# Optimization experiments

Measured on AMD Instinct MI355X. Metric: run time of the kernel, lower is better.

The kernel has to match this reference:

```python
import jax, jax.numpy as jnp
import numpy as np

THRESHOLD = 0.35
NEGPOS = 7
VAR0, VAR1 = 0.1, 0.2


def point_form(boxes):
    # (cx,cy,w,h) -> (x1,y1,x2,y2)
    return jnp.concatenate([boxes[:, :2] - boxes[:, 2:] / 2,
                            boxes[:, :2] + boxes[:, 2:] / 2], axis=1)


def jaccard(box_a, box_b):
    # box_a: [T,4], box_b: [P,4] in point form -> IoU [T,P]
    max_xy = jnp.minimum(box_a[:, None, 2:], box_b[None, :, 2:])
    min_xy = jnp.maximum(box_a[:, None, :2], box_b[None, :, :2])
    wh = jnp.clip(max_xy - min_xy, 0.0)
    inter = wh[..., 0] * wh[..., 1]
    area_a = ((box_a[:, 2] - box_a[:, 0]) * (box_a[:, 3] - box_a[:, 1]))[:, None]
    area_b = ((box_b[:, 2] - box_b[:, 0]) * (box_b[:, 3] - box_b[:, 1]))[None, :]
    return inter / (area_a + area_b - inter)


def encode(matched, priors):
    # matched: [P,4] point form, priors: [P,4] center form
    g_cxcy = ((matched[:, :2] + matched[:, 2:]) / 2 - priors[:, :2]) / (VAR0 * priors[:, 2:])
    g_wh = jnp.log((matched[:, 2:] - matched[:, :2]) / priors[:, 2:]) / VAR1
    return jnp.concatenate([g_cxcy, g_wh], axis=1)


def encode_landm(matched, priors):
    m = matched.reshape(-1, 5, 2)                       # [P,5,2]
    g = (m - priors[:, None, :2]) / (VAR0 * priors[:, None, 2:])
    return g.reshape(-1, 10)


def match_one(truths, labels, landms, priors):
    # truths [T,4], labels [T], landms [T,10], priors [P,4]
    overlaps = jaccard(truths, point_form(priors))       # [T,P]
    best_prior_idx = jnp.argmax(overlaps, axis=1)        # [T]
    best_truth_overlap = overlaps.max(axis=0)            # [P]
    best_truth_idx = jnp.argmax(overlaps, axis=0)        # [P]
    best_truth_overlap = best_truth_overlap.at[best_prior_idx].set(2.0)
    def body(j, bti):
        return bti.at[best_prior_idx[j]].set(j)
    best_truth_idx = jax.lax.fori_loop(0, truths.shape[0], body, best_truth_idx)
    conf = jnp.where(best_truth_overlap < THRESHOLD, 0.0, labels[best_truth_idx])
    loc = encode(truths[best_truth_idx], priors)
    landm = encode_landm(landms[best_truth_idx], priors)
    return loc, conf, landm


def smooth_l1(p, t):
    d = jnp.abs(p - t)
    return jnp.where(d < 1.0, 0.5 * d * d, d - 0.5)


def reference(loc_data, conf_data, landm_data, priors, targets):
    num, num_priors, _ = loc_data.shape
    truths = targets[:, :, :4]
    landms = targets[:, :, 4:14]
    labels = targets[:, :, 14]
    loc_t, conf_f, landm_t = jax.vmap(match_one, in_axes=(0, 0, 0, None))(
        truths, labels, landms, priors)
    conf_t = conf_f.astype(jnp.int32)                    # [num, P]

    poslands = conf_t > 0
    loss_landm = jnp.sum(smooth_l1(landm_data, landm_t) * poslands[..., None])

    pos = conf_t != 0
    loss_l = jnp.sum(smooth_l1(loc_data, loc_t) * pos[..., None])

    conf_t = jnp.where(pos, 1, conf_t)
    # per-prior CE: logsumexp - logit[target]
    ce = jax.nn.logsumexp(conf_data, axis=-1) - \
        jnp.take_along_axis(conf_data, conf_t[..., None], axis=-1)[..., 0]

    # hard negative mining: rank negatives by CE, keep top negpos*num_pos
    loss_rank = jnp.where(pos, 0.0, ce)
    loss_idx = jnp.argsort(-loss_rank, axis=1)
    idx_rank = jnp.argsort(loss_idx, axis=1)
    num_pos = pos.sum(axis=1)
    num_neg = jnp.clip(NEGPOS * num_pos, 0, num_priors - 1)
    neg = idx_rank < num_neg[:, None]

    sel = pos | neg
    loss_c = jnp.sum(ce * sel)

    N = jnp.maximum(num_pos.sum().astype(loc_data.dtype), 1.0)
    N1 = jnp.maximum(poslands.sum().astype(loc_data.dtype), 1.0)
    return loss_l / N, loss_c / N, loss_landm / N1


def setup_inputs() -> dict:
    key = jax.random.key(0)
    ks = jax.random.split(key, 8)
    N, T, P = 16, 48, 65536
    loc_data = jax.random.normal(ks[0], (N, P, 4), dtype=jnp.float32) * 0.1
    conf_data = jax.random.normal(ks[1], (N, P, 2), dtype=jnp.float32)
    landm_data = jax.random.normal(ks[2], (N, P, 10), dtype=jnp.float32) * 0.1
    # priors in (cx,cy,w,h), w,h > 0
    pc = jax.random.uniform(ks[3], (P, 2), minval=0.05, maxval=0.95)
    pwh = jax.random.uniform(ks[4], (P, 2), minval=0.04, maxval=0.3)
    priors = jnp.concatenate([pc, pwh], axis=1).astype(jnp.float32)
    # GT boxes: valid point-form (x1<x2, y1<y2)
    tc = jax.random.uniform(ks[5], (N, T, 2), minval=0.1, maxval=0.9)
    twh = jax.random.uniform(ks[6], (N, T, 2), minval=0.05, maxval=0.3)
    boxes = jnp.concatenate([tc - twh / 2, tc + twh / 2], axis=-1)
    lm = jax.random.uniform(ks[7], (N, T, 10))
    labels = jnp.ones((N, T, 1))
    targets = jnp.concatenate([boxes, lm, labels], axis=-1).astype(jnp.float32)
    return {"loc_data": loc_data, "conf_data": conf_data,
            "landm_data": landm_data, "priors": priors, "targets": targets}
```

## Files before the change

kernel.cpp:

```cpp
#include <hip/hip_runtime.h>

#define NP 65536
#define NT 48
#define TH 0.35f
#define PPT 2
#define KC_BX 128

#define PACKED_OFF 0
#define HIST_OFF   6144
#define NCPY 4
#define ZERO_BYTES 530432
#define NEGSUM_OFF 530432
#define PART_OFF   531456
#define LRANK_OFF  596992

__device__ __forceinline__ float sml1(float d) {
    float a = fabsf(d);
    return a < 1.f ? 0.5f * a * a : a - 0.5f;
}

__global__ __launch_bounds__(256) void kA(const float* __restrict__ priors,
                                          const float* __restrict__ targets,
                                          unsigned long long* __restrict__ packed) {
    const int chunk = blockIdx.x, tg = blockIdx.y, b = blockIdx.z;
    const float* tb = targets + ((size_t)b * NT + tg * 8) * 15;
    float tx1[8], ty1[8], tx2[8], ty2[8], ta[8];
#pragma unroll
    for (int j = 0; j < 8; j++) {
        tx1[j] = tb[j * 15 + 0]; ty1[j] = tb[j * 15 + 1];
        tx2[j] = tb[j * 15 + 2]; ty2[j] = tb[j * 15 + 3];
        ta[j] = (tx2[j] - tx1[j]) * (ty2[j] - ty1[j]);
    }
    const int pbase = chunk * 4096;
    float bi[8], bu[8]; unsigned int bp_[8];
#pragma unroll
    for (int j = 0; j < 8; j++) { bi[j] = 0.f; bu[j] = 1.f; bp_[j] = pbase + threadIdx.x; }
    const float4* P4 = reinterpret_cast<const float4*>(priors);
    for (int i = threadIdx.x; i < 4096; i += 256) {
        const int p = pbase + i;
        const float4 q = P4[p];
        const float px1 = q.x - q.z * 0.5f, py1 = q.y - q.w * 0.5f;
        const float px2 = q.x + q.z * 0.5f, py2 = q.y + q.w * 0.5f;
        const float areaB = (px2 - px1) * (py2 - py1);
#pragma unroll
        for (int j = 0; j < 8; j++) {
            float w = fminf(tx2[j], px2) - fmaxf(tx1[j], px1);
            float h = fminf(ty2[j], py2) - fmaxf(ty1[j], py1);
            w = fmaxf(w, 0.f); h = fmaxf(h, 0.f);
            float inter = w * h;
            float u = ta[j] + areaB - inter;
            if (inter * bu[j] > bi[j] * u) { bi[j] = inter; bu[j] = u; bp_[j] = (unsigned int)p; }
        }
    }
    __shared__ unsigned long long red[4][8];
    const int lane = threadIdx.x & 63, w = threadIdx.x >> 6;
#pragma unroll
    for (int j = 0; j < 8; j++) {
        float iou = bi[j] * __builtin_amdgcn_rcpf(bu[j]);
        unsigned long long key =
            ((unsigned long long)__float_as_uint(iou) << 32) | (unsigned long long)(~bp_[j]);
        for (int s = 32; s > 0; s >>= 1) {
            unsigned long long o = __shfl_down(key, s, 64);
            if (o > key) key = o;
        }
        if (lane == 0) red[w][j] = key;
    }
    __syncthreads();
    if (threadIdx.x < 8) {
        unsigned long long m = red[0][threadIdx.x];
#pragma unroll
        for (int i = 1; i < 4; i++) { unsigned long long o = red[i][threadIdx.x]; if (o > m) m = o; }
        atomicMax(&packed[(b * 6 + tg) * 8 + threadIdx.x], m);
    }
}

__global__ __launch_bounds__(256) void kC(
    const float* __restrict__ loc_data, const float* __restrict__ conf_data,
    const float* __restrict__ landm_data, const float* __restrict__ priors,
    const float* __restrict__ targets, const unsigned long long* __restrict__ packed,
    float* __restrict__ lrank, unsigned int* __restrict__ hist1c,
    float* __restrict__ part) {
    const int b = blockIdx.y;
    const int bx = blockIdx.x;
    const int p0 = (bx * 256 + threadIdx.x) * PPT;
    const int blockBase = bx * 256 * PPT;

    __shared__ float4 tbox[NT];
    __shared__ float tlab[NT];
    __shared__ float tlm[NT][10];
    __shared__ unsigned int hist[2048];
    __shared__ int ccnt;
    __shared__ int clp[NT], clt[NT];

    if (threadIdx.x == 0) ccnt = 0;
#pragma unroll
    for (int i = 0; i < 8; i++) hist[threadIdx.x + i * 256] = 0;
    for (int i = threadIdx.x; i < NT * 15; i += 256) {
        int t = i / 15, f = i - t * 15;
        float v = targets[((size_t)b * NT + t) * 15 + f];
        if (f < 4) reinterpret_cast<float*>(&tbox[t])[f] = v;
        else if (f < 14) tlm[t][f - 4] = v;
        else tlab[t] = v;
    }
    __syncthreads();
    if (threadIdx.x < NT) {
        int t = threadIdx.x;
        int cp = (int)(~(unsigned int)(packed[(b * 6 + (t >> 3)) * 8 + (t & 7)] & 0xFFFFFFFFull));
        if ((unsigned int)(cp - blockBase) < (unsigned int)(256 * PPT)) {
            int idx = atomicAdd(&ccnt, 1);
            clp[idx] = cp; clt[idx] = t;
        }
    }
    __syncthreads();

    float px1[PPT], py1[PPT], px2[PPT], py2[PPT], aB[PPT];
    float bi[PPT], bu[PPT]; int bt[PPT];
#pragma unroll
    for (int j = 0; j < PPT; j++) {
        float4 q = reinterpret_cast<const float4*>(priors)[p0 + j];
        px1[j] = q.x - q.z * 0.5f; py1[j] = q.y - q.w * 0.5f;
        px2[j] = q.x + q.z * 0.5f; py2[j] = q.y + q.w * 0.5f;
        aB[j] = (px2[j] - px1[j]) * (py2[j] - py1[j]);
        bi[j] = 0.f; bu[j] = 1.f; bt[j] = 0;
    }

    for (int t = 0; t < NT; t++) {
        float4 tb = tbox[t];
        float ta = (tb.z - tb.x) * (tb.w - tb.y);
#pragma unroll
        for (int j = 0; j < PPT; j++) {
            float w = fminf(tb.z, px2[j]) - fmaxf(tb.x, px1[j]);
            float h = fminf(tb.w, py2[j]) - fmaxf(tb.y, py1[j]);
            w = fmaxf(w, 0.f); h = fmaxf(h, 0.f);
            float inter = w * h;
            float u = ta + aB[j] - inter;
            if (inter * bu[j] > bi[j] * u) { bi[j] = inter; bu[j] = u; bt[j] = t; }
        }
    }
    bool clf[PPT];
#pragma unroll
    for (int j = 0; j < PPT; j++) clf[j] = false;
    for (int i = 0; i < ccnt; i++) {
        int cp = clp[i], ct = clt[i];
        unsigned int d = (unsigned int)(cp - p0);
        if (d < PPT) {
#pragma unroll
            for (int j = 0; j < PPT; j++) {
                if (d == (unsigned int)j) {
                    bt[j] = clf[j] ? max(bt[j], ct) : ct;
                    clf[j] = true;
                }
            }
        }
    }

    const float4 cf = reinterpret_cast<const float4*>(conf_data)[((size_t)b * NP + p0) >> 1];
    float cx[PPT] = {cf.x, cf.z};
    float cy[PPT] = {cf.y, cf.w};

    float sl = 0.f, slm = 0.f, cep = 0.f;
    int cp_ = 0, cpl_ = 0;
    float lr[PPT];
#pragma unroll
    for (int j = 0; j < PPT; j++) {
        const int btj = bt[j];
        const bool over = clf[j] || (bi[j] >= TH * bu[j]);
        const int confi = over ? (int)tlab[btj] : 0;
        const bool pos = (confi != 0);
        const bool posl = (confi > 0);
        float m = fmaxf(cx[j], cy[j]);
        float lse = m + __logf(__expf(cx[j] - m) + __expf(cy[j] - m));
        float ce = lse - (pos ? cy[j] : cx[j]);
        lr[j] = pos ? 0.f : fmaxf(ce, 0.f);
        atomicAdd(&hist[__float_as_uint(lr[j]) >> 20], 1u);
        if (pos) {
            cep += ce; cp_++;
            float4 q = reinterpret_cast<const float4*>(priors)[p0 + j];
            float4 tb = tbox[btj];
            float izi = 1.f / (0.1f * q.z), iwi = 1.f / (0.1f * q.w);
            float gcx = ((tb.x + tb.z) * 0.5f - q.x) * izi;
            float gcy = ((tb.y + tb.w) * 0.5f - q.y) * iwi;
            float gw = __logf((tb.z - tb.x) / q.z) * 5.f;
            float gh = __logf((tb.w - tb.y) / q.w) * 5.f;
            float4 ld = reinterpret_cast<const float4*>(loc_data)[(size_t)b * NP + p0 + j];
            sl += sml1(ld.x - gcx) + sml1(ld.y - gcy) + sml1(ld.z - gw) + sml1(ld.w - gh);
            if (posl) {
                cpl_++;
                const float* lmd = landm_data + ((size_t)b * NP + p0 + j) * 10;
#pragma unroll
                for (int i = 0; i < 5; i++) {
                    float gx = (tlm[btj][2 * i] - q.x) * izi;
                    float gy = (tlm[btj][2 * i + 1] - q.y) * iwi;
                    slm += sml1(lmd[2 * i] - gx) + sml1(lmd[2 * i + 1] - gy);
                }
            }
        }
    }
    *reinterpret_cast<float2*>(&lrank[(size_t)b * NP + p0]) = make_float2(lr[0], lr[1]);

    for (int s = 32; s > 0; s >>= 1) {
        sl += __shfl_down(sl, s, 64);
        slm += __shfl_down(slm, s, 64);
        cep += __shfl_down(cep, s, 64);
        cp_ += __shfl_down(cp_, s, 64);
        cpl_ += __shfl_down(cpl_, s, 64);
    }
    __shared__ float rf[12];
    __shared__ int ri[8];
    const int lane = threadIdx.x & 63, w = threadIdx.x >> 6;
    if (lane == 0) { rf[w] = sl; rf[4 + w] = slm; rf[8 + w] = cep; ri[w] = cp_; ri[4 + w] = cpl_; }
    __syncthreads();
    if (threadIdx.x == 0) {
        float a = 0, bb = 0, c = 0; int d = 0, e = 0;
        for (int i = 0; i < 4; i++) { a += rf[i]; bb += rf[4 + i]; c += rf[8 + i]; d += ri[i]; e += ri[4 + i]; }
        float* pp = part + ((size_t)b * KC_BX + bx) * 8;
        pp[0] = a; pp[1] = bb; pp[2] = c; pp[3] = (float)d; pp[4] = (float)e;
    }
    unsigned int* gh = hist1c + (((unsigned int)(bx & (NCPY - 1)) * 16 + b) << 11);
#pragma unroll
    for (int i = 0; i < 8; i++) {
        unsigned int c = hist[threadIdx.x + i * 256];
        if (c) atomicAdd(&gh[threadIdx.x + i * 256], c);
    }
}

__global__ __launch_bounds__(256) void kF(const float* __restrict__ lrank,
                                          const unsigned int* __restrict__ hist1c,
                                          const float* __restrict__ part,
                                          float* __restrict__ negsum) {
    const int b = blockIdx.x >> 4, slice = blockIdx.x & 15;
    __shared__ float pk[4];
    __shared__ unsigned int sh[2048];
    __shared__ unsigned int ps[256];
    __shared__ int sbin;
    __shared__ unsigned int sacc;
    __shared__ float wsum[4];

    {
        float v = (threadIdx.x < KC_BX)
                      ? part[((size_t)b * KC_BX + threadIdx.x) * 8 + 3] : 0.f;
        for (int s = 32; s > 0; s >>= 1) v += __shfl_down(v, s, 64);
        if ((threadIdx.x & 63) == 0) pk[threadIdx.x >> 6] = v;
    }
    for (int off = 0; off < 2048; off += 256) {
        unsigned int s = 0;
#pragma unroll
        for (int c = 0; c < NCPY; c++) s += hist1c[((c * 16 + b) << 11) + off + threadIdx.x];
        sh[off + threadIdx.x] = s;
    }
    __syncthreads();
    int k = 7 * (int)(pk[0] + pk[1] + 0.5f);
    if (k > NP - 1) k = NP - 1;
    if (k <= 0) { if (threadIdx.x == 0) negsum[blockIdx.x] = 0.f; return; }

    {
        unsigned int s = 0;
#pragma unroll
        for (int i = 0; i < 8; i++) s += sh[threadIdx.x * 8 + i];
        ps[threadIdx.x] = s;
    }
    __syncthreads();
    if (threadIdx.x == 0) {
        unsigned int kk = (unsigned int)k, acc = 0; int g = 255;
        for (; g > 0; --g) { unsigned int pg = ps[g]; if (acc + pg >= kk) break; acc += pg; }
        int bin = g * 8;
        for (int i = 7; i >= 0; --i) {
            unsigned int c = sh[g * 8 + i];
            if (acc + c >= kk) { bin = g * 8 + i; break; }
            acc += c;
        }
        sbin = bin; sacc = acc;
    }
    __syncthreads();
    const unsigned int b1 = (unsigned int)sbin;
    const float4* v4 = reinterpret_cast<const float4*>(lrank + (size_t)b * NP + slice * 4096);
    float sum = 0.f;
    for (int i = threadIdx.x; i < 1024; i += 256) {
        float4 x = v4[i];
        if ((__float_as_uint(x.x) >> 20) > b1) sum += x.x;
        if ((__float_as_uint(x.y) >> 20) > b1) sum += x.y;
        if ((__float_as_uint(x.z) >> 20) > b1) sum += x.z;
        if ((__float_as_uint(x.w) >> 20) > b1) sum += x.w;
    }
    for (int s = 32; s > 0; s >>= 1) sum += __shfl_down(sum, s, 64);
    const int lane = threadIdx.x & 63, w = threadIdx.x >> 6;
    if (lane == 0) wsum[w] = sum;
    __syncthreads();
    if (threadIdx.x == 0) {
        float tot = wsum[0] + wsum[1] + wsum[2] + wsum[3];
        if (slice == 0) {
            unsigned int k2 = (unsigned int)k - sacc;
            tot += (float)k2 * __uint_as_float((b1 << 20) | 0x80000u);
        }
        negsum[blockIdx.x] = tot;
    }
}

__global__ __launch_bounds__(1024) void kE(const float* __restrict__ part,
                                           const float* __restrict__ negsum,
                                           float* __restrict__ out) {
    float sl = 0.f, slm = 0.f, cep = 0.f, cp = 0.f, cpl = 0.f;
#pragma unroll
    for (int r = 0; r < 2; r++) {
        const float* pp = part + ((size_t)threadIdx.x + r * 1024) * 8;
        sl += pp[0]; slm += pp[1]; cep += pp[2]; cp += pp[3]; cpl += pp[4];
    }
    float ns = (threadIdx.x < 256) ? negsum[threadIdx.x] : 0.f;
    for (int s = 32; s > 0; s >>= 1) {
        sl += __shfl_down(sl, s, 64);
        slm += __shfl_down(slm, s, 64);
        cep += __shfl_down(cep, s, 64);
        cp += __shfl_down(cp, s, 64);
        cpl += __shfl_down(cpl, s, 64);
        ns += __shfl_down(ns, s, 64);
    }
    __shared__ float r_[16][6];
    const int lane = threadIdx.x & 63, w = threadIdx.x >> 6;
    if (lane == 0) {
        r_[w][0] = sl; r_[w][1] = slm; r_[w][2] = cep;
        r_[w][3] = cp; r_[w][4] = cpl; r_[w][5] = ns;
    }
    __syncthreads();
    if (threadIdx.x == 0) {
        float a = 0, bb = 0, c = 0, d = 0, e = 0, n = 0;
        for (int i = 0; i < 16; i++) {
            a += r_[i][0]; bb += r_[i][1]; c += r_[i][2];
            d += r_[i][3]; e += r_[i][4]; n += r_[i][5];
        }
        float N = fmaxf(d, 1.f);
        float N1 = fmaxf(e, 1.f);
        out[0] = a / N;
        out[1] = (c + n) / N;
        out[2] = bb / N1;
    }
}

extern "C" void kernel_launch(void* const* d_in, const int* in_sizes, int n_in,
                              void* d_out, int out_size, void* d_ws, size_t ws_size,
                              hipStream_t stream) {
    const float* loc_data = (const float*)d_in[0];
    const float* conf_data = (const float*)d_in[1];
    const float* landm_data = (const float*)d_in[2];
    const float* priors = (const float*)d_in[3];
    const float* targets = (const float*)d_in[4];
    float* out = (float*)d_out;
    char* ws = (char*)d_ws;
    unsigned long long* packed = (unsigned long long*)(ws + PACKED_OFF);
    unsigned int* hist1c = (unsigned int*)(ws + HIST_OFF);
    float* negsum = (float*)(ws + NEGSUM_OFF);
    float* part = (float*)(ws + PART_OFF);
    float* lrank = (float*)(ws + LRANK_OFF);

    hipMemsetAsync(ws, 0, ZERO_BYTES, stream);
    kA<<<dim3(16, 6, 16), 256, 0, stream>>>(priors, targets, packed);
    kC<<<dim3(KC_BX, 16), 256, 0, stream>>>(loc_data, conf_data, landm_data, priors, targets,
                                            packed, lrank, hist1c, part);
    kF<<<256, 256, 0, stream>>>(lrank, hist1c, part, negsum);
    kE<<<1, 1024, 0, stream>>>(part, negsum, out);
}
```

Baseline: 171.2 us.

## Replace lrank buffer with per-bin sum histograms and drop memset via per-chunk maxima

```diff
diff --git a/kernel.cpp b/kernel.cpp
--- a/kernel.cpp
+++ b/kernel.cpp
@@ -5,14 +5,15 @@
 #define TH 0.35f
 #define PPT 2
 #define KC_BX 128
-
-#define PACKED_OFF 0
-#define HIST_OFF   6144
+#define NCHUNK 16
 #define NCPY 4
-#define ZERO_BYTES 530432
-#define NEGSUM_OFF 530432
-#define PART_OFF   531456
-#define LRANK_OFF  596992
+
+#define PERCHUNK_OFF 0
+#define HISTC_OFF    98304
+#define HISTS_OFF    622592
+#define NEGSUM_OFF   1146880
+#define PART_OFF     1147136
+#define HIST_DWORDS  262144
 
 __device__ __forceinline__ float sml1(float d) {
     float a = fabsf(d);
@@ -21,8 +22,14 @@
 
 __global__ __launch_bounds__(256) void kA(const float* __restrict__ priors,
                                           const float* __restrict__ targets,
-                                          unsigned long long* __restrict__ packed) {
+                                          unsigned long long* __restrict__ perchunk,
+                                          unsigned int* __restrict__ histz) {
     const int chunk = blockIdx.x, tg = blockIdx.y, b = blockIdx.z;
+    {
+        int flat = (b * 6 + tg) * NCHUNK + chunk;
+        int base = flat * 171 + (int)threadIdx.x;
+        if (threadIdx.x < 171 && base < HIST_DWORDS) histz[base] = 0u;
+    }
     const float* tb = targets + ((size_t)b * NT + tg * 8) * 15;
     float tx1[8], ty1[8], tx2[8], ty2[8], ta[8];
 #pragma unroll
@@ -32,9 +39,9 @@
         ta[j] = (tx2[j] - tx1[j]) * (ty2[j] - ty1[j]);
     }
     const int pbase = chunk * 4096;
-    float bi[8], bu[8]; unsigned int bp_[8];
-#pragma unroll
-    for (int j = 0; j < 8; j++) { bi[j] = 0.f; bu[j] = 1.f; bp_[j] = pbase + threadIdx.x; }
+    float bi[8], bs[8]; unsigned int bp_[8];
+#pragma unroll
+    for (int j = 0; j < 8; j++) { bi[j] = 0.f; bs[j] = 1.f; bp_[j] = pbase + threadIdx.x; }
     const float4* P4 = reinterpret_cast<const float4*>(priors);
     for (int i = threadIdx.x; i < 4096; i += 256) {
         const int p = pbase + i;
@@ -48,15 +55,16 @@
             float h = fminf(ty2[j], py2) - fmaxf(ty1[j], py1);
             w = fmaxf(w, 0.f); h = fmaxf(h, 0.f);
             float inter = w * h;
-            float u = ta[j] + areaB - inter;
-            if (inter * bu[j] > bi[j] * u) { bi[j] = inter; bu[j] = u; bp_[j] = (unsigned int)p; }
+            float S = ta[j] + areaB;
+            if (inter * bs[j] > bi[j] * S) { bi[j] = inter; bs[j] = S; bp_[j] = (unsigned int)p; }
         }
     }
     __shared__ unsigned long long red[4][8];
     const int lane = threadIdx.x & 63, w = threadIdx.x >> 6;
 #pragma unroll
     for (int j = 0; j < 8; j++) {
-        float iou = bi[j] * __builtin_amdgcn_rcpf(bu[j]);
+        float bu = bs[j] - bi[j];
+        float iou = bi[j] / bu;
         unsigned long long key =
             ((unsigned long long)__float_as_uint(iou) << 32) | (unsigned long long)(~bp_[j]);
         for (int s = 32; s > 0; s >>= 1) {
@@ -70,15 +78,15 @@
         unsigned long long m = red[0][threadIdx.x];
 #pragma unroll
         for (int i = 1; i < 4; i++) { unsigned long long o = red[i][threadIdx.x]; if (o > m) m = o; }
-        atomicMax(&packed[(b * 6 + tg) * 8 + threadIdx.x], m);
+        perchunk[((size_t)b * NT + tg * 8 + threadIdx.x) * NCHUNK + chunk] = m;
     }
 }
 
 __global__ __launch_bounds__(256) void kC(
     const float* __restrict__ loc_data, const float* __restrict__ conf_data,
     const float* __restrict__ landm_data, const float* __restrict__ priors,
-    const float* __restrict__ targets, const unsigned long long* __restrict__ packed,
-    float* __restrict__ lrank, unsigned int* __restrict__ hist1c,
+    const float* __restrict__ targets, const unsigned long long* __restrict__ perchunk,
+    unsigned int* __restrict__ hist_cnt, float* __restrict__ hist_sum,
     float* __restrict__ part) {
     const int b = blockIdx.y;
     const int bx = blockIdx.x;
@@ -88,13 +96,14 @@
     __shared__ float4 tbox[NT];
     __shared__ float tlab[NT];
     __shared__ float tlm[NT][10];
-    __shared__ unsigned int hist[2048];
+    __shared__ unsigned int hcnt[2048];
+    __shared__ float hsum[2048];
     __shared__ int ccnt;
     __shared__ int clp[NT], clt[NT];
 
     if (threadIdx.x == 0) ccnt = 0;
 #pragma unroll
-    for (int i = 0; i < 8; i++) hist[threadIdx.x + i * 256] = 0;
+    for (int i = 0; i < 8; i++) { hcnt[threadIdx.x + i * 256] = 0; hsum[threadIdx.x + i * 256] = 0.f; }
     for (int i = threadIdx.x; i < NT * 15; i += 256) {
         int t = i / 15, f = i - t * 15;
         float v = targets[((size_t)b * NT + t) * 15 + f];
@@ -104,24 +113,27 @@
     }
     __syncthreads();
     if (threadIdx.x < NT) {
-        int t = threadIdx.x;
-        int cp = (int)(~(unsigned int)(packed[(b * 6 + (t >> 3)) * 8 + (t & 7)] & 0xFFFFFFFFull));
+        const unsigned long long* pk = perchunk + ((size_t)b * NT + threadIdx.x) * NCHUNK;
+        unsigned long long m = pk[0];
+#pragma unroll
+        for (int c = 1; c < NCHUNK; c++) { unsigned long long o = pk[c]; if (o > m) m = o; }
+        int cp = (int)(~(unsigned int)(m & 0xFFFFFFFFull));
         if ((unsigned int)(cp - blockBase) < (unsigned int)(256 * PPT)) {
             int idx = atomicAdd(&ccnt, 1);
-            clp[idx] = cp; clt[idx] = t;
+            clp[idx] = cp; clt[idx] = threadIdx.x;
         }
     }
     __syncthreads();
 
     float px1[PPT], py1[PPT], px2[PPT], py2[PPT], aB[PPT];
-    float bi[PPT], bu[PPT]; int bt[PPT];
+    float bi[PPT], bs[PPT]; int bt[PPT];
 #pragma unroll
     for (int j = 0; j < PPT; j++) {
         float4 q = reinterpret_cast<const float4*>(priors)[p0 + j];
         px1[j] = q.x - q.z * 0.5f; py1[j] = q.y - q.w * 0.5f;
         px2[j] = q.x + q.z * 0.5f; py2[j] = q.y + q.w * 0.5f;
         aB[j] = (px2[j] - px1[j]) * (py2[j] - py1[j]);
-        bi[j] = 0.f; bu[j] = 1.f; bt[j] = 0;
+        bi[j] = 0.f; bs[j] = 1.f; bt[j] = 0;
     }
 
     for (int t = 0; t < NT; t++) {
@@ -133,8 +145,8 @@
             float h = fminf(tb.w, py2[j]) - fmaxf(tb.y, py1[j]);
             w = fmaxf(w, 0.f); h = fmaxf(h, 0.f);
             float inter = w * h;
-            float u = ta + aB[j] - inter;
-            if (inter * bu[j] > bi[j] * u) { bi[j] = inter; bu[j] = u; bt[j] = t; }
+            float S = ta + aB[j];
+            if (inter * bs[j] > bi[j] * S) { bi[j] = inter; bs[j] = S; bt[j] = t; }
         }
     }
     bool clf[PPT];
@@ -160,19 +172,20 @@
 
     float sl = 0.f, slm = 0.f, cep = 0.f;
     int cp_ = 0, cpl_ = 0;
-    float lr[PPT];
 #pragma unroll
     for (int j = 0; j < PPT; j++) {
         const int btj = bt[j];
-        const bool over = clf[j] || (bi[j] >= TH * bu[j]);
+        const bool over = clf[j] || (bi[j] >= TH * (bs[j] - bi[j]));
         const int confi = over ? (int)tlab[btj] : 0;
         const bool pos = (confi != 0);
         const bool posl = (confi > 0);
         float m = fmaxf(cx[j], cy[j]);
         float lse = m + __logf(__expf(cx[j] - m) + __expf(cy[j] - m));
         float ce = lse - (pos ? cy[j] : cx[j]);
-        lr[j] = pos ? 0.f : fmaxf(ce, 0.f);
-        atomicAdd(&hist[__float_as_uint(lr[j]) >> 20], 1u);
+        float lr = pos ? 0.f : fmaxf(ce, 0.f);
+        unsigned int bin = __float_as_uint(lr) >> 20;
+        atomicAdd(&hcnt[bin], 1u);
+        if (lr != 0.f) atomicAdd(&hsum[bin], lr);
         if (pos) {
             cep += ce; cp_++;
             float4 q = reinterpret_cast<const float4*>(priors)[p0 + j];
@@ -196,7 +209,6 @@
             }
         }
     }
-    *reinterpret_cast<float2*>(&lrank[(size_t)b * NP + p0]) = make_float2(lr[0], lr[1]);
 
     for (int s = 32; s > 0; s >>= 1) {
         sl += __shfl_down(sl, s, 64);
@@ -216,21 +228,28 @@
         float* pp = part + ((size_t)b * KC_BX + bx) * 8;
         pp[0] = a; pp[1] = bb; pp[2] = c; pp[3] = (float)d; pp[4] = (float)e;
     }
-    unsigned int* gh = hist1c + (((unsigned int)(bx & (NCPY - 1)) * 16 + b) << 11);
-#pragma unroll
-    for (int i = 0; i < 8; i++) {
-        unsigned int c = hist[threadIdx.x + i * 256];
-        if (c) atomicAdd(&gh[threadIdx.x + i * 256], c);
-    }
-}
-
-__global__ __launch_bounds__(256) void kF(const float* __restrict__ lrank,
-                                          const unsigned int* __restrict__ hist1c,
+    {
+        const unsigned int cidx = ((unsigned int)(bx & (NCPY - 1)) * 16 + b) << 11;
+        unsigned int* gc = hist_cnt + cidx;
+        float* gs = hist_sum + cidx;
+#pragma unroll
+        for (int i = 0; i < 8; i++) {
+            unsigned int c = hcnt[threadIdx.x + i * 256];
+            if (c) atomicAdd(&gc[threadIdx.x + i * 256], c);
+            float s = hsum[threadIdx.x + i * 256];
+            if (s != 0.f) atomicAdd(&gs[threadIdx.x + i * 256], s);
+        }
+    }
+}
+
+__global__ __launch_bounds__(256) void kF(const unsigned int* __restrict__ hist_cnt,
+                                          const float* __restrict__ hist_sum,
                                           const float* __restrict__ part,
                                           float* __restrict__ negsum) {
-    const int b = blockIdx.x >> 4, slice = blockIdx.x & 15;
-    __shared__ float pk[4];
-    __shared__ unsigned int sh[2048];
+    const int b = blockIdx.x;
+    __shared__ float pk[2];
+    __shared__ unsigned int shc[2048];
+    __shared__ float shs[2048];
     __shared__ unsigned int ps[256];
     __shared__ int sbin;
     __shared__ unsigned int sacc;
@@ -240,23 +259,28 @@
         float v = (threadIdx.x < KC_BX)
                       ? part[((size_t)b * KC_BX + threadIdx.x) * 8 + 3] : 0.f;
         for (int s = 32; s > 0; s >>= 1) v += __shfl_down(v, s, 64);
-        if ((threadIdx.x & 63) == 0) pk[threadIdx.x >> 6] = v;
+        if ((threadIdx.x & 63) == 0 && threadIdx.x < 128) pk[threadIdx.x >> 6] = v;
     }
     for (int off = 0; off < 2048; off += 256) {
-        unsigned int s = 0;
-#pragma unroll
-        for (int c = 0; c < NCPY; c++) s += hist1c[((c * 16 + b) << 11) + off + threadIdx.x];
-        sh[off + threadIdx.x] = s;
+        unsigned int c = 0; float s = 0.f;
+#pragma unroll
+        for (int cp = 0; cp < NCPY; cp++) {
+            unsigned int idx = (((unsigned int)cp * 16 + b) << 11) + off + threadIdx.x;
+            c += hist_cnt[idx];
+            s += hist_sum[idx];
+        }
+        shc[off + threadIdx.x] = c;
+        shs[off + threadIdx.x] = s;
     }
     __syncthreads();
     int k = 7 * (int)(pk[0] + pk[1] + 0.5f);
     if (k > NP - 1) k = NP - 1;
-    if (k <= 0) { if (threadIdx.x == 0) negsum[blockIdx.x] = 0.f; return; }
+    if (k <= 0) { if (threadIdx.x == 0) negsum[b] = 0.f; return; }
 
     {
         unsigned int s = 0;
 #pragma unroll
-        for (int i = 0; i < 8; i++) s += sh[threadIdx.x * 8 + i];
+        for (int i = 0; i < 8; i++) s += shc[threadIdx.x * 8 + i];
         ps[threadIdx.x] = s;
     }
     __syncthreads();
@@ -265,34 +289,26 @@
         for (; g > 0; --g) { unsigned int pg = ps[g]; if (acc + pg >= kk) break; acc += pg; }
         int bin = g * 8;
         for (int i = 7; i >= 0; --i) {
-            unsigned int c = sh[g * 8 + i];
+            unsigned int c = shc[g * 8 + i];
             if (acc + c >= kk) { bin = g * 8 + i; break; }
             acc += c;
         }
         sbin = bin; sacc = acc;
     }
     __syncthreads();
-    const unsigned int b1 = (unsigned int)sbin;
-    const float4* v4 = reinterpret_cast<const float4*>(lrank + (size_t)b * NP + slice * 4096);
+    const int b1 = sbin;
     float sum = 0.f;
-    for (int i = threadIdx.x; i < 1024; i += 256) {
-        float4 x = v4[i];
-        if ((__float_as_uint(x.x) >> 20) > b1) sum += x.x;
-        if ((__float_as_uint(x.y) >> 20) > b1) sum += x.y;
-        if ((__float_as_uint(x.z) >> 20) > b1) sum += x.z;
-        if ((__float_as_uint(x.w) >> 20) > b1) sum += x.w;
-    }
+    for (int i = threadIdx.x; i < 2048; i += 256)
+        if (i > b1) sum += shs[i];
     for (int s = 32; s > 0; s >>= 1) sum += __shfl_down(sum, s, 64);
     const int lane = threadIdx.x & 63, w = threadIdx.x >> 6;
     if (lane == 0) wsum[w] = sum;
     __syncthreads();
     if (threadIdx.x == 0) {
         float tot = wsum[0] + wsum[1] + wsum[2] + wsum[3];
-        if (slice == 0) {
-            unsigned int k2 = (unsigned int)k - sacc;
-            tot += (float)k2 * __uint_as_float((b1 << 20) | 0x80000u);
-        }
-        negsum[blockIdx.x] = tot;
+        unsigned int k2 = (unsigned int)k - sacc;
+        tot += (float)k2 * __uint_as_float(((unsigned int)b1 << 20) | 0x80000u);
+        negsum[b] = tot;
     }
 }
 
@@ -305,7 +321,7 @@
         const float* pp = part + ((size_t)threadIdx.x + r * 1024) * 8;
         sl += pp[0]; slm += pp[1]; cep += pp[2]; cp += pp[3]; cpl += pp[4];
     }
-    float ns = (threadIdx.x < 256) ? negsum[threadIdx.x] : 0.f;
+    float ns = (threadIdx.x < 16) ? negsum[threadIdx.x] : 0.f;
     for (int s = 32; s > 0; s >>= 1) {
         sl += __shfl_down(sl, s, 64);
         slm += __shfl_down(slm, s, 64);
@@ -345,16 +361,15 @@
     const float* targets = (const float*)d_in[4];
     float* out = (float*)d_out;
     char* ws = (char*)d_ws;
-    unsigned long long* packed = (unsigned long long*)(ws + PACKED_OFF);
-    unsigned int* hist1c = (unsigned int*)(ws + HIST_OFF);
+    unsigned long long* perchunk = (unsigned long long*)(ws + PERCHUNK_OFF);
+    unsigned int* hist_cnt = (unsigned int*)(ws + HISTC_OFF);
+    float* hist_sum = (float*)(ws + HISTS_OFF);
     float* negsum = (float*)(ws + NEGSUM_OFF);
     float* part = (float*)(ws + PART_OFF);
-    float* lrank = (float*)(ws + LRANK_OFF);
-
-    hipMemsetAsync(ws, 0, ZERO_BYTES, stream);
-    kA<<<dim3(16, 6, 16), 256, 0, stream>>>(priors, targets, packed);
+
+    kA<<<dim3(NCHUNK, 6, 16), 256, 0, stream>>>(priors, targets, perchunk, hist_cnt);
     kC<<<dim3(KC_BX, 16), 256, 0, stream>>>(loc_data, conf_data, landm_data, priors, targets,
-                                            packed, lrank, hist1c, part);
-    kF<<<256, 256, 0, stream>>>(lrank, hist1c, part, negsum);
+                                            perchunk, hist_cnt, hist_sum, part);
+    kF<<<16, 256, 0, stream>>>(hist_cnt, hist_sum, part, negsum);
     kE<<<1, 1024, 0, stream>>>(part, negsum, out);
 }
```

Result: slower. 175.1 us (+2.3%).
